# Kernel tuning notes

Hardware: AMD Instinct MI355X
Metric: run time of the kernel (lower is better)

The kernel has to match this reference:

```python
import jax, jax.numpy as jnp
import numpy as np

H = 768
NH = 12
HD = H // NH


def setup_inputs() -> dict:
    key = jax.random.key(0)
    ks = jax.random.split(key, 12)
    B, S = 2, 2048
    s = 1.0 / np.sqrt(H)
    inp = {
        "hidden_states": jax.random.normal(ks[0], (B, S, H), dtype=jnp.float32),
        "attention_mask": jnp.ones((B, S), dtype=jnp.float32),
        "Wq": jax.random.normal(ks[1], (H, H), dtype=jnp.float32) * s,
        "bq": jnp.zeros((H,), dtype=jnp.float32),
        "Wk": jax.random.normal(ks[2], (H, H), dtype=jnp.float32) * s,
        "bk": jnp.zeros((H,), dtype=jnp.float32),
        "Wv": jax.random.normal(ks[3], (H, H), dtype=jnp.float32) * s,
        "bv": jnp.zeros((H,), dtype=jnp.float32),
        "Wo": jax.random.normal(ks[4], (H, H), dtype=jnp.float32) * s,
        "bo": jnp.zeros((H,), dtype=jnp.float32),
        "ln_gamma": jnp.ones((H,), dtype=jnp.float32),
        "ln_beta": jnp.zeros((H,), dtype=jnp.float32),
    }
    return inp


def _split_heads(x):
    # [B,S,H] -> [B,NH,S,HD]
    B, S, _ = x.shape
    return x.reshape(B, S, NH, HD).transpose(0, 2, 1, 3)


def reference(hidden_states, attention_mask, Wq, bq, Wk, bk, Wv, bv, Wo, bo, ln_gamma, ln_beta):
    x = hidden_states
    q = _split_heads(x @ Wq.T + bq)
    k = _split_heads(x @ Wk.T + bk)
    v = _split_heads(x @ Wv.T + bv)
    # scores: [B,NH,S,S]
    scores = jnp.einsum("bhqd,bhkd->bhqk", q, k) / jnp.sqrt(jnp.float32(HD))
    mask = (1.0 - attention_mask)[:, None, None, :] * -10000.0
    scores = scores + mask
    probs = jax.nn.softmax(scores, axis=-1)  # dropout is identity at inference
    ctx = jnp.einsum("bhqk,bhkd->bhqd", probs, v)
    B, _, S, _ = ctx.shape
    ctx = ctx.transpose(0, 2, 1, 3).reshape(B, S, H)
    out = ctx @ Wo.T + bo
    y = out + x
    mu = jnp.mean(y, axis=-1, keepdims=True)
    var = jnp.var(y, axis=-1, keepdims=True)
    y = (y - mu) / jnp.sqrt(var + 1e-5)
    return y * ln_gamma + ln_beta
```

## Files before the change

kernel.cpp:

```cpp
#include <hip/hip_runtime.h>
#include <math.h>

#define HH 768
#define NHEADS 12
#define HDIM 64
#define SEQ 2048
#define NB 2
#define L2E 1.44269504088896f

typedef __attribute__((ext_vector_type(8))) short s8v;
typedef __attribute__((ext_vector_type(4))) short s4v;
typedef __attribute__((ext_vector_type(4))) float f4v;

static __device__ inline short f2bf(float f) {
    union { float f; unsigned u; } v; v.f = f;
    unsigned r = v.u + 0x7fff + ((v.u >> 16) & 1);
    return (short)(r >> 16);
}

#if __has_builtin(__builtin_amdgcn_exp2f)
#define EXP2(x) __builtin_amdgcn_exp2f(x)
#else
#define EXP2(x) __expf((x) * 0.6931471805599453f)
#endif

__device__ __forceinline__ unsigned cvt_pk_bf16(float a, float b) {
    unsigned r;
    asm("v_cvt_pk_bf16_f32 %0, %1, %2" : "=v"(r) : "v"(a), "v"(b));
    return r;
}

__device__ __forceinline__ void gld16(const void* g, void* l) {
    __builtin_amdgcn_global_load_lds(
        (const __attribute__((address_space(1))) void*)g,
        (__attribute__((address_space(3))) void*)l, 16, 0, 0);
}

__device__ __forceinline__ int kperm(int k) {
    return (k & ~31) | (((k >> 2) & 3) << 3) | (((k >> 4) & 1) << 2) | (k & 3);
}

#define XV8   393216
#define WV8   73728
__global__ __launch_bounds__(256)
void cvt_kernel(const float* __restrict__ X, short* __restrict__ Xb,
                const float* __restrict__ W0, short* __restrict__ W0b,
                const float* __restrict__ W1, short* __restrict__ W1b,
                const float* __restrict__ W2, short* __restrict__ W2b,
                const float* __restrict__ W3, short* __restrict__ W3b)
{
    int gid = blockIdx.x * 256 + threadIdx.x;
    const float* src; short* dst; size_t off;
    if      (gid < XV8)            { src = X;  dst = Xb;  off = gid; }
    else if (gid < XV8 + WV8)      { src = W0; dst = W0b; off = gid - XV8; }
    else if (gid < XV8 + 2*WV8)    { src = W1; dst = W1b; off = gid - XV8 - WV8; }
    else if (gid < XV8 + 3*WV8)    { src = W2; dst = W2b; off = gid - XV8 - 2*WV8; }
    else if (gid < XV8 + 4*WV8)    { src = W3; dst = W3b; off = gid - XV8 - 3*WV8; }
    else return;
    off *= 8;
    float4 a = *(const float4*)(src + off);
    float4 b = *(const float4*)(src + off + 4);
    s8v o;
    o[0] = f2bf(a.x); o[1] = f2bf(a.y); o[2] = f2bf(a.z); o[3] = f2bf(a.w);
    o[4] = f2bf(b.x); o[5] = f2bf(b.y); o[6] = f2bf(b.z); o[7] = f2bf(b.w);
    *(s8v*)(dst + off) = o;
}

template<int EPI>
__global__ __launch_bounds__(256)
void gemm_mfma(const short* __restrict__ A,
               const short* __restrict__ Wq, const short* __restrict__ Wk,
               const short* __restrict__ Wv,
               const float* __restrict__ bq, const float* __restrict__ bk,
               const float* __restrict__ bv,
               short* __restrict__ Qo, short* __restrict__ Ko, short* __restrict__ Vo,
               const float* __restrict__ Xres, float* __restrict__ Fo)
{
    __shared__ __align__(16) short As[64*32];
    __shared__ __align__(16) short Bs[128*32];

    const int tid  = threadIdx.x;
    const int w    = tid >> 6;
    const int lane = tid & 63;
    const int g    = lane >> 4;
    const int r    = lane & 15;
    const int wr   = w >> 1;
    const int wc   = w & 1;

    const int NBX = (EPI == 0) ? 18 : 6;
    const int NXB = (EPI == 0) ? 144 : 48;
    const int wg  = (blockIdx.x & 7) * NXB + (blockIdx.x >> 3);
    const int bx  = wg % NBX;
    const int by  = wg / NBX;
    const int m0  = by * 64;

    int n0;
    int seg = 0;
    const short* Wb; const float* bias; short* outp; float scale;
    if (EPI == 0) {
        seg = bx / 6;
        n0 = (bx % 6) * 128;
        Wb   = seg == 0 ? Wq : seg == 1 ? Wk : Wv;
        bias = seg == 0 ? bq : seg == 1 ? bk : bv;
        outp = seg == 0 ? Qo : seg == 1 ? Ko : Vo;
        scale = seg == 0 ? (0.125f * L2E) : 1.0f;
    } else {
        n0 = bx * 128;
        Wb = Wq; bias = bq; outp = nullptr; scale = 1.0f;
    }

    const int srow = tid >> 2;
    const int scol = (tid & 3) * 8;
    const short* Asrc  = A  + (size_t)(m0 + srow) * HH + scol;
    const short* Bsrc0 = Wb + (size_t)(n0 + srow) * HH + scol;
    const short* Bsrc1 = Wb + (size_t)(n0 + 64 + srow) * HH + scol;
    short* Ald  = As + w*512;
    short* Bld0 = Bs + w*512;
    short* Bld1 = Bs + 2048 + w*512;

    f4v acc[2][4];
    #pragma unroll
    for (int i = 0; i < 2; i++)
        #pragma unroll
        for (int j = 0; j < 4; j++) acc[i][j] = (f4v){0.f,0.f,0.f,0.f};

    for (int kt = 0; kt < HH/32; ++kt) {
        const int k0 = kt * 32;
        gld16(Asrc  + k0, Ald);
        gld16(Bsrc0 + k0, Bld0);
        gld16(Bsrc1 + k0, Bld1);
        __syncthreads();

        s8v af[2], bf[4];
        #pragma unroll
        for (int mi = 0; mi < 2; mi++)
            af[mi] = *(const s8v*)(As + (wr*32 + mi*16 + r)*32 + g*8);
        #pragma unroll
        for (int ni = 0; ni < 4; ni++)
            bf[ni] = *(const s8v*)(Bs + (wc*64 + ni*16 + r)*32 + g*8);
        __builtin_amdgcn_s_setprio(1);
        #pragma unroll
        for (int mi = 0; mi < 2; mi++)
            #pragma unroll
            for (int ni = 0; ni < 4; ni++)
                acc[mi][ni] = __builtin_amdgcn_mfma_f32_16x16x32_bf16(af[mi], bf[ni], acc[mi][ni], 0, 0, 0);
        __builtin_amdgcn_s_setprio(0);
        __syncthreads();
    }

    if (EPI == 0) {
        if (seg < 2) {
            #pragma unroll
            for (int mi = 0; mi < 2; mi++) {
                #pragma unroll
                for (int j = 0; j < 4; j++) {
                    const int m = m0 + wr*32 + mi*16 + 4*g + j;
                    const int bb = m >> 11;
                    const int s  = m & 2047;
                    #pragma unroll
                    for (int ni = 0; ni < 4; ni++) {
                        const int n = n0 + wc*64 + ni*16 + r;
                        const int h = n >> 6;
                        const int d = n & 63;
                        outp[((size_t)((bb*NHEADS + h)*SEQ) + s)*HDIM + d] =
                            f2bf((acc[mi][ni][j] + bias[n]) * scale);
                    }
                }
            }
        } else {
            #pragma unroll
            for (int mi = 0; mi < 2; mi++) {
                const int m  = m0 + wr*32 + mi*16 + 4*g;
                const int bb = m >> 11;
                const int s  = m & 2047;
                const int sp = kperm(s);
                #pragma unroll
                for (int ni = 0; ni < 4; ni++) {
                    const int n = n0 + wc*64 + ni*16 + r;
                    const int h = n >> 6;
                    const int d = n & 63;
                    s4v pk;
                    #pragma unroll
                    for (int j = 0; j < 4; j++)
                        pk[j] = f2bf(acc[mi][ni][j] + bias[n]);
                    *(s4v*)(outp + ((size_t)((bb*NHEADS + h)*HDIM) + d)*SEQ + sp) = pk;
                }
            }
        }
    } else {
        #pragma unroll
        for (int mi = 0; mi < 2; mi++) {
            #pragma unroll
            for (int j = 0; j < 4; j++) {
                const int m = m0 + wr*32 + mi*16 + 4*g + j;
                #pragma unroll
                for (int ni = 0; ni < 4; ni++) {
                    const int n = n0 + wc*64 + ni*16 + r;
                    Fo[(size_t)m*HH + n] = acc[mi][ni][j] + bias[n] + Xres[(size_t)m*HH + n];
                }
            }
        }
    }
}

#define NPAIR (SEQ/64)
__global__ __launch_bounds__(512, 4)
void attn_mfma(const short* __restrict__ Q, const short* __restrict__ K,
               const short* __restrict__ VT, const float* __restrict__ mask,
               short* __restrict__ CTX)
{
    const int wgid = (blockIdx.x & 7) * 96 + (blockIdx.x >> 3);
    const int qt = wgid & 31;
    const int bh = wgid >> 5;
    const int h  = bh % NHEADS;
    const int b  = bh / NHEADS;

    const size_t hb = (size_t)(b * NHEADS + h);
    const short* Qg  = Q  + hb * SEQ * HDIM;
    const short* Kg  = K  + hb * SEQ * HDIM;
    const short* VTg = VT + hb * HDIM * SEQ;

    __shared__ __align__(16) char lds[40960];
    char* Kbase = lds;
    char* Vbase = lds + 16384;
    float* Mf   = (float*)(lds + 32768);

    const int tid  = threadIdx.x;
    const int w    = tid >> 6;
    const int grp  = w >> 2;
    const int wq   = w & 3;
    const int lane = tid & 63;
    const int g    = lane >> 4;
    const int r    = lane & 15;
    const int q0   = qt * 64;

    const short* qrow = Qg + (size_t)(q0 + wq*16 + r) * HDIM;
    const s8v qf0 = *(const s8v*)(qrow + 8*g);
    const s8v qf1 = *(const s8v*)(qrow + 8*g + 32);

    {
        float4 mv = *(const float4*)(mask + b*SEQ + tid*4);
        f4v md;
        md[0] = (mv.x - 1.0f) * (10000.0f * L2E);
        md[1] = (mv.y - 1.0f) * (10000.0f * L2E);
        md[2] = (mv.z - 1.0f) * (10000.0f * L2E);
        md[3] = (mv.w - 1.0f) * (10000.0f * L2E);
        *(f4v*)(Mf + kperm(tid*4)) = md;
    }

    f4v acc[4];
    #pragma unroll
    for (int t = 0; t < 4; t++) acc[t] = (f4v){0.f, 0.f, 0.f, 0.f};
    float lpart = 0.0f;

    const int srow = lane >> 3;
    const int scol = 8 * ((lane & 7) ^ srow);

    #define STAGE(PT, DB) do {                                                 \
        const int pk0 = (PT) * 64;                                             \
        char* kd = Kbase + (DB)*8192 + w*1024;                                 \
        gld16(Kg + (size_t)(pk0 + 8*w + srow)*HDIM + scol, kd);                \
        char* vd = Vbase + (DB)*8192 + w*1024;                                 \
        gld16(VTg + (size_t)(8*w + srow)*SEQ + pk0 + scol, vd);                \
    } while (0)

    STAGE(0, 0);
    __syncthreads();

    for (int pt = 0; pt < NPAIR; ++pt) {
        const int db = pt & 1;
        if (pt + 1 < NPAIR) STAGE(pt + 1, db ^ 1);

        const char* Kc = Kbase + db*8192 + grp*4096;
        const char* Vc = Vbase + db*8192;

        const float* mrow = Mf + pt*64 + grp*32 + 8*g;
        f4v z0 = *(const f4v*)(mrow);
        f4v z1 = *(const f4v*)(mrow + 4);

        __builtin_amdgcn_s_setprio(1);
        {
            const int sw = (r & 7) << 4;
            const char* kb0 = Kc + r * 128;
            const char* kb1 = Kc + (16 + r) * 128;
            s8v ka0 = *(const s8v*)(kb0 + ((16*g)      ^ sw));
            s8v ka1 = *(const s8v*)(kb0 + ((16*g + 64) ^ sw));
            s8v kc0 = *(const s8v*)(kb1 + ((16*g)      ^ sw));
            s8v kc1 = *(const s8v*)(kb1 + ((16*g + 64) ^ sw));
            z0 = __builtin_amdgcn_mfma_f32_16x16x32_bf16(ka0, qf0, z0, 0, 0, 0);
            z0 = __builtin_amdgcn_mfma_f32_16x16x32_bf16(ka1, qf1, z0, 0, 0, 0);
            z1 = __builtin_amdgcn_mfma_f32_16x16x32_bf16(kc0, qf0, z1, 0, 0, 0);
            z1 = __builtin_amdgcn_mfma_f32_16x16x32_bf16(kc1, qf1, z1, 0, 0, 0);
        }
        __builtin_amdgcn_s_setprio(0);

        #pragma unroll
        for (int i = 0; i < 4; i++) {
            z0[i] = EXP2(z0[i]);
            z1[i] = EXP2(z1[i]);
        }
        lpart += ((z0[0] + z0[1]) + (z0[2] + z0[3]))
               + ((z1[0] + z1[1]) + (z1[2] + z1[3]));

        union { unsigned u[4]; s8v v; } pfu;
        pfu.u[0] = cvt_pk_bf16(z0[0], z0[1]);
        pfu.u[1] = cvt_pk_bf16(z0[2], z0[3]);
        pfu.u[2] = cvt_pk_bf16(z1[0], z1[1]);
        pfu.u[3] = cvt_pk_bf16(z1[2], z1[3]);
        const s8v pf = pfu.v;

        __builtin_amdgcn_s_setprio(1);
        #pragma unroll
        for (int t4 = 0; t4 < 4; t4++) {
            const int vrow = 16*t4 + r;
            s8v vf = *(const s8v*)(Vc + vrow*128 + ((16*(4*grp + g)) ^ ((r & 7) << 4)));
            acc[t4] = __builtin_amdgcn_mfma_f32_16x16x32_bf16(pf, vf, acc[t4], 0, 0, 0);
        }
        __builtin_amdgcn_s_setprio(0);

        __syncthreads();
    }

    lpart += __shfl_xor(lpart, 16);
    lpart += __shfl_xor(lpart, 32);

    float* lbuf = (float*)(lds + 20480);
    if (grp == 1) {
        float* mb = (float*)(lds + wq*5120 + lane*80);
        *(f4v*)(mb)      = acc[0];
        *(f4v*)(mb + 4)  = acc[1];
        *(f4v*)(mb + 8)  = acc[2];
        *(f4v*)(mb + 12) = acc[3];
        lbuf[wq*64 + lane] = lpart;
    }
    __syncthreads();
    if (grp == 0) {
        const float* mb = (const float*)(lds + wq*5120 + lane*80);
        acc[0] += *(const f4v*)(mb);
        acc[1] += *(const f4v*)(mb + 4);
        acc[2] += *(const f4v*)(mb + 8);
        acc[3] += *(const f4v*)(mb + 12);
        lpart  += lbuf[wq*64 + lane];

        #pragma unroll
        for (int i = 0; i < 4; i++) {
            const float invl = 1.0f / __shfl(lpart, 4*g + i);
            const size_t rowbase = ((size_t)(b*SEQ) + q0 + wq*16 + 4*g + i) * HH + h*HDIM;
            #pragma unroll
            for (int t4 = 0; t4 < 4; t4++)
                CTX[rowbase + 16*t4 + r] = f2bf(acc[t4][i] * invl);
        }
    }
    #undef STAGE
}

__global__ __launch_bounds__(256)
void ln_kernel(float* __restrict__ y, const float* __restrict__ gamma,
               const float* __restrict__ beta)
{
    const int row = blockIdx.x;
    float* p = y + (size_t)row * HH;
    const int tid = threadIdx.x;

    float v[3];
    float s = 0.f, ss = 0.f;
    #pragma unroll
    for (int i = 0; i < 3; i++) {
        float x = p[tid + i*256];
        v[i] = x;
        s += x;
        ss += x * x;
    }
    #pragma unroll
    for (int off = 32; off > 0; off >>= 1) {
        s  += __shfl_down(s,  off);
        ss += __shfl_down(ss, off);
    }
    __shared__ float sbuf[4], ssbuf[4];
    __shared__ float mu_s, rstd_s;
    const int wave = tid >> 6;
    if ((tid & 63) == 0) { sbuf[wave] = s; ssbuf[wave] = ss; }
    __syncthreads();
    if (tid == 0) {
        float S  = sbuf[0] + sbuf[1] + sbuf[2] + sbuf[3];
        float SS = ssbuf[0] + ssbuf[1] + ssbuf[2] + ssbuf[3];
        float mu = S * (1.0f / HH);
        float var = SS * (1.0f / HH) - mu * mu;
        mu_s = mu;
        rstd_s = rsqrtf(var + 1e-5f);
    }
    __syncthreads();
    const float mu = mu_s, rstd = rstd_s;
    #pragma unroll
    for (int i = 0; i < 3; i++) {
        const int c = tid + i*256;
        p[c] = (v[i] - mu) * rstd * gamma[c] + beta[c];
    }
}

extern "C" void kernel_launch(void* const* d_in, const int* in_sizes, int n_in,
                              void* d_out, int out_size, void* d_ws, size_t ws_size,
                              hipStream_t stream)
{
    const float* x     = (const float*)d_in[0];
    const float* mask  = (const float*)d_in[1];
    const float* Wq    = (const float*)d_in[2];
    const float* bq    = (const float*)d_in[3];
    const float* Wk    = (const float*)d_in[4];
    const float* bk    = (const float*)d_in[5];
    const float* Wv    = (const float*)d_in[6];
    const float* bv    = (const float*)d_in[7];
    const float* Wo    = (const float*)d_in[8];
    const float* bo    = (const float*)d_in[9];
    const float* gamma = (const float*)d_in[10];
    const float* beta  = (const float*)d_in[11];

    const size_t PER = (size_t)NB * NHEADS * SEQ * HDIM;
    const size_t WSZ = (size_t)HH * HH;
    short* wsS  = (short*)d_ws;
    short* Xb   = wsS;
    short* Wqb  = wsS + PER;
    short* Wkb  = Wqb + WSZ;
    short* Wvb  = Wkb + WSZ;
    short* Wob  = Wvb + WSZ;
    short* Qb   = Wob + WSZ;
    short* Kb   = Qb + PER;
    short* VTb  = Kb + PER;
    short* CTXb = Xb;
    float* out  = (float*)d_out;

    cvt_kernel<<<2688, 256, 0, stream>>>(x, Xb, Wq, Wqb, Wk, Wkb, Wv, Wvb, Wo, Wob);

    gemm_mfma<0><<<1152, 256, 0, stream>>>(
        Xb, Wqb, Wkb, Wvb, bq, bk, bv, Qb, Kb, VTb, nullptr, nullptr);

    attn_mfma<<<768, 512, 0, stream>>>(Qb, Kb, VTb, mask, CTXb);

    gemm_mfma<1><<<384, 256, 0, stream>>>(
        CTXb, Wob, nullptr, nullptr, bo, nullptr, nullptr,
        nullptr, nullptr, nullptr, x, out);

    ln_kernel<<<NB*SEQ, 256, 0, stream>>>(out, gamma, beta);
}
```

Before: 100.4 us.

## Double-buffer GEMM LDS tiles and XOR-swizzle columns to avoid bank conflicts

The projection GEMM now keeps two LDS stages and issues the global-to-LDS loads for the next k-tile before computing the current one, with a single barrier per iteration. This is meant to overlap load latency with MFMA work. It also XOR-swizzles the 8-element column slot by row so the fragment reads hit different LDS banks. LDS use per block doubles, which may lower occupancy, and correctness depends on the asynchronous loads landing before the barrier.

```diff
diff --git a/kernel.cpp b/kernel.cpp
--- a/kernel.cpp
+++ b/kernel.cpp
@@ -66,6 +66,7 @@
     *(s8v*)(dst + off) = o;
 }
 
+#define NKT (HH/32)
 template<int EPI>
 __global__ __launch_bounds__(256)
 void gemm_mfma(const short* __restrict__ A,
@@ -76,8 +77,8 @@
                short* __restrict__ Qo, short* __restrict__ Ko, short* __restrict__ Vo,
                const float* __restrict__ Xres, float* __restrict__ Fo)
 {
-    __shared__ __align__(16) short As[64*32];
-    __shared__ __align__(16) short Bs[128*32];
+    __shared__ __align__(16) short As[2*64*32];
+    __shared__ __align__(16) short Bs[2*128*32];
 
     const int tid  = threadIdx.x;
     const int w    = tid >> 6;
@@ -110,13 +111,16 @@
     }
 
     const int srow = tid >> 2;
-    const int scol = (tid & 3) * 8;
+    const int scol = 8 * ((tid & 3) ^ (srow & 3));
     const short* Asrc  = A  + (size_t)(m0 + srow) * HH + scol;
     const short* Bsrc0 = Wb + (size_t)(n0 + srow) * HH + scol;
     const short* Bsrc1 = Wb + (size_t)(n0 + 64 + srow) * HH + scol;
-    short* Ald  = As + w*512;
-    short* Bld0 = Bs + w*512;
-    short* Bld1 = Bs + 2048 + w*512;
+
+    #define GSTAGE(KT, DB) do { const int k0 = (KT) * 32;                      \
+        gld16(Asrc  + k0, As + (DB)*2048 + w*512);                             \
+        gld16(Bsrc0 + k0, Bs + (DB)*4096 + w*512);                             \
+        gld16(Bsrc1 + k0, Bs + (DB)*4096 + 2048 + w*512);                      \
+    } while (0)
 
     f4v acc[2][4];
     #pragma unroll
@@ -124,20 +128,23 @@
         #pragma unroll
         for (int j = 0; j < 4; j++) acc[i][j] = (f4v){0.f,0.f,0.f,0.f};
 
-    for (int kt = 0; kt < HH/32; ++kt) {
-        const int k0 = kt * 32;
-        gld16(Asrc  + k0, Ald);
-        gld16(Bsrc0 + k0, Bld0);
-        gld16(Bsrc1 + k0, Bld1);
-        __syncthreads();
-
+    GSTAGE(0, 0);
+    __syncthreads();
+
+    for (int kt = 0; kt < NKT; ++kt) {
+        const int db = kt & 1;
+        if (kt + 1 < NKT) GSTAGE(kt + 1, db ^ 1);
+
+        const short* Ab = As + db*2048;
+        const short* Bb = Bs + db*4096;
+        const int slot = (g ^ (r & 3)) * 8;
         s8v af[2], bf[4];
         #pragma unroll
         for (int mi = 0; mi < 2; mi++)
-            af[mi] = *(const s8v*)(As + (wr*32 + mi*16 + r)*32 + g*8);
+            af[mi] = *(const s8v*)(Ab + (wr*32 + mi*16 + r)*32 + slot);
         #pragma unroll
         for (int ni = 0; ni < 4; ni++)
-            bf[ni] = *(const s8v*)(Bs + (wc*64 + ni*16 + r)*32 + g*8);
+            bf[ni] = *(const s8v*)(Bb + (wc*64 + ni*16 + r)*32 + slot);
         __builtin_amdgcn_s_setprio(1);
         #pragma unroll
         for (int mi = 0; mi < 2; mi++)
@@ -145,6 +152,7 @@
             for (int ni = 0; ni < 4; ni++)
                 acc[mi][ni] = __builtin_amdgcn_mfma_f32_16x16x32_bf16(af[mi], bf[ni], acc[mi][ni], 0, 0, 0);
         __builtin_amdgcn_s_setprio(0);
+
         __syncthreads();
     }
 
@@ -201,6 +209,7 @@
             }
         }
     }
+    #undef GSTAGE
 }
 
 #define NPAIR (SEQ/64)
```

Result: no change. 102.2 us (+1.8%).
